# Optimization experiments

Hardware: AMD Instinct MI355X
Metric: run time of the kernel (lower is better)

Reference implementation:

```python
import jax, jax.numpy as jnp
import numpy as np

C2 = 256.0  # self.C = float(c2); softmax scale = 1/sqrt(C2)

def setup_inputs() -> dict:
    key = jax.random.key(0)
    k1, k2, k3, k4 = jax.random.split(key, 4)
    fm = jax.random.normal(k1, (1, 256, 96, 96), dtype=jnp.float32)
    ft = jax.random.normal(k2, (1, 256, 96, 96), dtype=jnp.float32)
    # 1x1 conv: in_channels = 2*256 = 512, out_channels = 256
    theta_w = jax.random.normal(k3, (256, 512, 1, 1), dtype=jnp.float32) * 0.04
    theta_b = jax.random.normal(k4, (256,), dtype=jnp.float32) * 0.01
    return {"fm": fm, "ft": ft, "theta_w": theta_w, "theta_b": theta_b}

def reference(fm, ft, theta_w, theta_b):
    B, C, H, W = fm.shape
    B1, C1, H1, W1 = ft.shape
    # torch .view(C, B*H*W) on a contiguous [B,C,H,W] tensor == row-major reshape
    fm_r = fm.reshape(C, B * H * W)          # [C, N]
    ft_r = ft.reshape(C1, B1 * H1 * W1)      # [C, M]
    scale = 1.0 / jnp.sqrt(jnp.float32(C2))
    S = jnp.einsum('cn,cm->nm', fm_r, ft_r) * scale   # [N, M]
    w = jax.nn.softmax(S, axis=-1)
    fm_weighted = jnp.einsum('cn,nm->cm', fm_r, w)    # [C, M]
    fm_attended = fm_weighted.reshape(B1, C1, H1, W1)
    cat = jnp.concatenate([fm_attended, ft], axis=1)  # [B1, 2*C1, H1, W1]
    # 1x1 conv
    out = jnp.einsum('oc,bchw->bohw', theta_w[:, :, 0, 0], cat) + theta_b[None, :, None, None]
    return out
```

## Files before the change

### kernel.cpp

```cpp
#include <hip/hip_runtime.h>

#define NHW 9216
#define NCH 256
#define SCALE 0.0625f

typedef __attribute__((ext_vector_type(8))) short bfrag;
typedef __attribute__((ext_vector_type(4))) float f32x4;
typedef __attribute__((ext_vector_type(8))) unsigned short u16x8;
typedef __attribute__((address_space(3))) unsigned as3_u32;
typedef const __attribute__((address_space(1))) unsigned as1_u32;

__device__ __forceinline__ unsigned short f2bf(float x) {
    unsigned u = __builtin_bit_cast(unsigned, x);
    u += 0x7FFFu + ((u >> 16) & 1u);
    return (unsigned short)(u >> 16);
}

#define MFMA(a, b, c) __builtin_amdgcn_mfma_f32_16x16x32_bf16((a), (b), (c), 0, 0, 0)

__global__ __launch_bounds__(256) void k_prep(const float* __restrict__ fm,
                                              const float* __restrict__ ft,
                                              unsigned short* __restrict__ fmT,
                                              unsigned short* __restrict__ ftT) {
    __shared__ float smT[64][257];
    const float* src = blockIdx.y ? ft : fm;
    unsigned short* dst = blockIdx.y ? ftT : fmT;
    const int t = threadIdx.x;
    const int n0 = blockIdx.x * 64;
    {
        const int n = t & 63;
        const int cb = t >> 6;
        for (int p = 0; p < 64; ++p) {
            const int c = p * 4 + cb;
            smT[n][c] = src[(size_t)c * NHW + n0 + n];
        }
    }
    __syncthreads();
    {
        const int n = t >> 2;
        const int c0 = (t & 3) * 64;
#pragma unroll
        for (int cc = 0; cc < 64; cc += 8) {
            const float4 v0 = *(const float4*)(&smT[n][c0 + cc]);
            const float4 v1 = *(const float4*)(&smT[n][c0 + cc + 4]);
            u16x8 o;
            o[0] = f2bf(v0.x); o[1] = f2bf(v0.y); o[2] = f2bf(v0.z); o[3] = f2bf(v0.w);
            o[4] = f2bf(v1.x); o[5] = f2bf(v1.y); o[6] = f2bf(v1.z); o[7] = f2bf(v1.w);
            *(u16x8*)(dst + (size_t)(n0 + n) * NCH + c0 + cc) = o;
        }
    }
}

__global__ __launch_bounds__(256) void k_prepw(const float* __restrict__ tw,
                                               unsigned short* __restrict__ twb) {
    const int i = blockIdx.x * 256 + threadIdx.x;
    twb[i] = f2bf(tw[i]);
}

__global__ __launch_bounds__(256, 2) void k_se(const unsigned short* __restrict__ fmT,
                                               const unsigned short* __restrict__ ftT,
                                               float* __restrict__ Zpart,
                                               unsigned short* __restrict__ E,
                                               int storeE) {
    __shared__ unsigned short smB[2][16384];
    const int t = threadIdx.x;
    const int w = t >> 6, l = t & 63;
    const int lr = l & 15, lk = l >> 4;
    const int id = blockIdx.x;
    const int by = id & 15;
    const int bx = id >> 4;
    const int n0 = bx * 128 + w * 32;
    const int mb = by * 576;

    bfrag a[2][8];
#pragma unroll
    for (int i = 0; i < 2; ++i)
#pragma unroll
        for (int ks = 0; ks < 8; ++ks)
            a[i][ks] = *(const bfrag*)(fmT + (size_t)(n0 + i * 16 + lr) * NCH + ks * 32 + lk * 8);

    float zacc[2][4] = {};
    f32x4 accA[2][4], accB[2][4];

#define STAGE(buf, mt)                                                                   \
    {                                                                                    \
        const int sm0 = mb + (mt) * 64;                                                  \
        _Pragma("unroll") for (int p = 0; p < 8; ++p) {                                  \
            const int chunkb = p * 256 + w * 64;                                         \
            const int chunk = chunkb + l;                                                \
            const int m = chunk >> 5;                                                    \
            const int scb = (chunk & 31) ^ (m & 7);                                      \
            const unsigned short* gp = ftT + (size_t)(sm0 + m) * NCH + scb * 8;          \
            unsigned short* lp = &smB[buf][0] + (size_t)chunk * 8;                       \
            __builtin_amdgcn_global_load_lds((as1_u32*)gp, (as3_u32*)lp, 16, 0, 0);      \
        }                                                                                \
    }

#define COMPUTE(acc, buf)                                                                \
    {                                                                                    \
        _Pragma("unroll") for (int i = 0; i < 2; ++i)                                    \
            _Pragma("unroll") for (int j = 0; j < 4; ++j) acc[i][j] = (f32x4){0,0,0,0};  \
        _Pragma("unroll") for (int ks = 0; ks < 8; ++ks) {                               \
            bfrag b[4];                                                                  \
            _Pragma("unroll") for (int j = 0; j < 4; ++j) {                              \
                const int mloc = j * 16 + lr;                                            \
                const int cb = ks * 4 + lk;                                              \
                b[j] = *(const bfrag*)(&smB[buf][mloc * 256 + ((cb ^ (mloc & 7)) << 3)]);\
            }                                                                            \
            _Pragma("unroll") for (int i = 0; i < 2; ++i)                                \
                _Pragma("unroll") for (int j = 0; j < 4; ++j)                            \
                    acc[i][j] = MFMA(a[i][ks], b[j], acc[i][j]);                         \
        }                                                                                \
    }

#define EXPSTORE(acc, mt)                                                                \
    {                                                                                    \
        const int sm0 = mb + (mt) * 64;                                                  \
        _Pragma("unroll") for (int i = 0; i < 2; ++i) {                                  \
            const int grp = (n0 + i * 16 + lk * 4) >> 3;                                 \
            const int sub = (lk & 1) * 4;                                                \
            _Pragma("unroll") for (int j = 0; j < 4; ++j) {                              \
                float e0 = __expf(acc[i][j][0] * SCALE);                                 \
                float e1 = __expf(acc[i][j][1] * SCALE);                                 \
                float e2 = __expf(acc[i][j][2] * SCALE);                                 \
                float e3 = __expf(acc[i][j][3] * SCALE);                                 \
                zacc[i][0] += e0; zacc[i][1] += e1;                                      \
                zacc[i][2] += e2; zacc[i][3] += e3;                                      \
                if (storeE) {                                                            \
                    const int m = sm0 + j * 16 + lr;                                     \
                    uint2 v;                                                             \
                    v.x = (unsigned)f2bf(e0) | ((unsigned)f2bf(e1) << 16);               \
                    v.y = (unsigned)f2bf(e2) | ((unsigned)f2bf(e3) << 16);               \
                    *(uint2*)(&E[((size_t)grp * NHW + m) * 8 + sub]) = v;                \
                }                                                                        \
            }                                                                            \
        }                                                                                \
    }

    STAGE(0, 0)
    __syncthreads();
    STAGE(1, 1)
    COMPUTE(accA, 0)
    __syncthreads();
    for (int base = 1; base + 1 < 9; base += 2) {
        STAGE(0, base + 1)
        EXPSTORE(accA, base - 1)
        COMPUTE(accB, 1)
        __syncthreads();
        if (base + 2 < 9) STAGE(1, base + 2)
        EXPSTORE(accB, base)
        COMPUTE(accA, 0)
        __syncthreads();
    }
    EXPSTORE(accA, 8)
#undef STAGE
#undef COMPUTE
#undef EXPSTORE

#pragma unroll
    for (int i = 0; i < 2; ++i)
#pragma unroll
        for (int r = 0; r < 4; ++r) {
            float v = zacc[i][r];
            v += __shfl_xor(v, 1);
            v += __shfl_xor(v, 2);
            v += __shfl_xor(v, 4);
            v += __shfl_xor(v, 8);
            if (lr == 0) Zpart[(size_t)by * NHW + n0 + i * 16 + lk * 4 + r] = v;
        }
}

__global__ __launch_bounds__(256) void k_gb(const unsigned short* __restrict__ twb,
                                            const unsigned short* __restrict__ fmT,
                                            const unsigned short* __restrict__ ftT,
                                            const float* __restrict__ Zpart,
                                            const float* __restrict__ tb,
                                            unsigned short* __restrict__ G,
                                            float* __restrict__ out) {
    const int tid = threadIdx.x;
    const int w = tid >> 6, l = tid & 63;
    const int wo = w >> 1, wm = w & 1;
    const int lr = l & 15, lk = l >> 4;
    const int mode = blockIdx.z;
    const int n0 = blockIdx.x * 128, o0 = blockIdx.y * 128;
    const unsigned short* B = mode ? ftT : fmT;
    const int wofs = mode ? 256 : 0;
    f32x4 acc[4][4] = {};
#pragma unroll
    for (int ks = 0; ks < 8; ++ks) {
        const int k = ks * 32 + lk * 8;
        bfrag a[4], b[4];
#pragma unroll
        for (int i = 0; i < 4; ++i)
            a[i] = *(const bfrag*)(twb + (size_t)(o0 + wo * 64 + i * 16 + lr) * 512 + wofs + k);
#pragma unroll
        for (int j = 0; j < 4; ++j)
            b[j] = *(const bfrag*)(B + (size_t)(n0 + wm * 64 + j * 16 + lr) * NCH + k);
#pragma unroll
        for (int i = 0; i < 4; ++i)
#pragma unroll
            for (int j = 0; j < 4; ++j) acc[i][j] = MFMA(a[i], b[j], acc[i][j]);
    }
    if (mode == 0) {
        float zi[4];
#pragma unroll
        for (int j = 0; j < 4; ++j) {
            const int n = n0 + wm * 64 + j * 16 + lr;
            float z = 0.f;
#pragma unroll
            for (int s = 0; s < 16; ++s) z += Zpart[(size_t)s * NHW + n];
            zi[j] = 1.f / z;
        }
#pragma unroll
        for (int i = 0; i < 4; ++i)
#pragma unroll
            for (int j = 0; j < 4; ++j)
#pragma unroll
                for (int r = 0; r < 4; ++r) {
                    const int o = o0 + wo * 64 + i * 16 + lk * 4 + r;
                    const int n = n0 + wm * 64 + j * 16 + lr;
                    G[(size_t)(n >> 3) * 2048 + o * 8 + (n & 7)] = f2bf(acc[i][j][r] * zi[j]);
                }
    } else {
#pragma unroll
        for (int i = 0; i < 4; ++i)
#pragma unroll
            for (int j = 0; j < 4; ++j)
#pragma unroll
                for (int r = 0; r < 4; ++r) {
                    const int o = o0 + wo * 64 + i * 16 + lk * 4 + r;
                    const int m = n0 + wm * 64 + j * 16 + lr;
                    out[(size_t)o * NHW + m] = acc[i][j][r] + tb[o];
                }
    }
}

__global__ __launch_bounds__(256, 3) void k_apply(const unsigned short* __restrict__ G,
                                                  const unsigned short* __restrict__ E,
                                                  float* __restrict__ out) {
    const int t = threadIdx.x;
    const int w = t >> 6, l = t & 63;
    const int lr = l & 15, lk = l >> 4;
    const int id = blockIdx.x;
    const int by = id & 7;
    const int bx = id >> 3;
    const int m0 = bx * 64;
    const int gbase = by * 144;

    f32x4 U[4][4] = {};
    bfrag gaA[4], ebA[4], gaB[4], ebB[4];

#define LOADSET(ga, eb, s)                                                                        \
    {                                                                                             \
        _Pragma("unroll") for (int i = 0; i < 4; ++i)                                             \
            ga[i] = *(const bfrag*)(&G[(size_t)(gbase + (s) * 4 + lk) * 2048 +                    \
                                       (w * 64 + i * 16 + lr) * 8]);                              \
        _Pragma("unroll") for (int j = 0; j < 4; ++j)                                             \
            eb[j] = *(const bfrag*)(&E[((size_t)(gbase + (s) * 4 + lk) * NHW + m0 + j * 16 + lr) * 8]); \
    }
#define MFMASET(ga, eb)                                                                           \
    {                                                                                             \
        _Pragma("unroll") for (int i = 0; i < 4; ++i)                                             \
            _Pragma("unroll") for (int j = 0; j < 4; ++j) U[i][j] = MFMA(ga[i], eb[j], U[i][j]);  \
    }

    LOADSET(gaA, ebA, 0)
#pragma unroll 2
    for (int s = 0; s < 36; s += 2) {
        LOADSET(gaB, ebB, s + 1)
        MFMASET(gaA, ebA)
        if (s + 2 < 36) LOADSET(gaA, ebA, s + 2)
        MFMASET(gaB, ebB)
    }
#undef LOADSET
#undef MFMASET

#pragma unroll
    for (int i = 0; i < 4; ++i)
#pragma unroll
        for (int j = 0; j < 4; ++j)
#pragma unroll
            for (int r = 0; r < 4; ++r) {
                const int o = w * 64 + i * 16 + lk * 4 + r;
                const int m = m0 + j * 16 + lr;
                atomicAdd(out + (size_t)o * NHW + m, U[i][j][r]);
            }
}

__global__ __launch_bounds__(256, 2) void k_main(const unsigned short* __restrict__ fmT,
                                                 const unsigned short* __restrict__ ftT,
                                                 const unsigned short* __restrict__ G,
                                                 float* __restrict__ out) {
    __shared__ unsigned short smB[32 * 64 * 8];
    __shared__ unsigned short smE[48 * 64 * 8];
    const int t = threadIdx.x;
    const int w = t >> 6, l = t & 63;
    const int lr = l & 15, lk = l >> 4;
    const int id = blockIdx.x;
    const int by = id & 7;
    const int bx = id >> 3;
    const int m0 = bx * 64;
    const int nbase = by * 1152;

    {
        const int m = t >> 2;
        const int kc0 = t & 3;
#pragma unroll
        for (int p = 0; p < 8; ++p) {
            const int kc = p * 4 + kc0;
            *(bfrag*)(&smB[(kc * 64 + m) * 8]) =
                *(const bfrag*)(ftT + (size_t)(m0 + m) * NCH + kc * 8);
        }
    }
    __syncthreads();

    f32x4 U[4][4] = {};
    for (int c = 0; c < 3; ++c) {
        const int n0 = nbase + c * 384;
        f32x4 acc[6][4] = {};
#pragma unroll
        for (int ks = 0; ks < 8; ++ks) {
            const int k = ks * 32 + lk * 8;
            bfrag a[6], b[4];
#pragma unroll
            for (int i = 0; i < 6; ++i)
                a[i] = *(const bfrag*)(fmT + (size_t)(n0 + w * 96 + i * 16 + lr) * NCH + k);
#pragma unroll
            for (int j = 0; j < 4; ++j)
                b[j] = *(const bfrag*)(&smB[((ks * 4 + lk) * 64 + j * 16 + lr) * 8]);
#pragma unroll
            for (int i = 0; i < 6; ++i)
#pragma unroll
                for (int j = 0; j < 4; ++j) acc[i][j] = MFMA(a[i], b[j], acc[i][j]);
        }
#pragma unroll
        for (int i = 0; i < 6; ++i)
#pragma unroll
            for (int j = 0; j < 4; ++j) {
                const int m = j * 16 + lr;
                const int grp = w * 12 + i * 2 + (lk >> 1);
                uint2 v;
                v.x = (unsigned)f2bf(__expf(acc[i][j][0] * SCALE)) |
                      ((unsigned)f2bf(__expf(acc[i][j][1] * SCALE)) << 16);
                v.y = (unsigned)f2bf(__expf(acc[i][j][2] * SCALE)) |
                      ((unsigned)f2bf(__expf(acc[i][j][3] * SCALE)) << 16);
                *(uint2*)(&smE[(grp * 64 + m) * 8 + (lk & 1) * 4]) = v;
            }
        __syncthreads();
#pragma unroll
        for (int s = 0; s < 12; ++s) {
            bfrag ga[4], eb[4];
#pragma unroll
            for (int i = 0; i < 4; ++i)
                ga[i] = *(const bfrag*)(&G[(size_t)((n0 + s * 32 + lk * 8) >> 3) * 2048 +
                                           (w * 64 + i * 16 + lr) * 8]);
#pragma unroll
            for (int j = 0; j < 4; ++j)
                eb[j] = *(const bfrag*)(&smE[((s * 4 + lk) * 64 + j * 16 + lr) * 8]);
#pragma unroll
            for (int i = 0; i < 4; ++i)
#pragma unroll
                for (int j = 0; j < 4; ++j) U[i][j] = MFMA(ga[i], eb[j], U[i][j]);
        }
        __syncthreads();
    }
#pragma unroll
    for (int i = 0; i < 4; ++i)
#pragma unroll
        for (int j = 0; j < 4; ++j)
#pragma unroll
            for (int r = 0; r < 4; ++r) {
                const int o = w * 64 + i * 16 + lk * 4 + r;
                const int m = m0 + j * 16 + lr;
                atomicAdd(out + (size_t)o * NHW + m, U[i][j][r]);
            }
}

extern "C" void kernel_launch(void* const* d_in, const int* in_sizes, int n_in,
                              void* d_out, int out_size, void* d_ws, size_t ws_size,
                              hipStream_t stream) {
    const float* fm = (const float*)d_in[0];
    const float* ft = (const float*)d_in[1];
    const float* tw = (const float*)d_in[2];
    const float* tb = (const float*)d_in[3];
    float* out = (float*)d_out;

    char* ws = (char*)d_ws;
    float* Zpart = (float*)ws;
    unsigned short* twb = (unsigned short*)(ws + 589824);
    unsigned short* fmT = (unsigned short*)(ws + 851968);
    unsigned short* ftT = (unsigned short*)(ws + 5570560);
    unsigned short* G   = (unsigned short*)(ws + 10289152);
    unsigned short* E   = (unsigned short*)(ws + 15007744);
    const size_t needE = 15007744ull + (size_t)NHW * NHW * 2ull;
    const int useE = (ws_size >= needE) ? 1 : 0;

    k_prep<<<dim3(144, 2), 256, 0, stream>>>(fm, ft, fmT, ftT);
    k_prepw<<<dim3(512), 256, 0, stream>>>(tw, twb);
    k_se<<<dim3(1152), 256, 0, stream>>>(fmT, ftT, Zpart, E, useE);
    k_gb<<<dim3(72, 2, 2), 256, 0, stream>>>(twb, fmT, ftT, Zpart, tb, G, out);
    if (useE)
        k_apply<<<dim3(1152), 256, 0, stream>>>(G, E, out);
    else
        k_main<<<dim3(1152), 256, 0, stream>>>(fmT, ftT, G, out);
}
```

Measured before the change: 199.5 us.

## Stage G and E tiles through LDS with async loads and wider M tile

k_apply now copies G and E tiles into double-buffered shared memory using global_load_lds, and computes from LDS instead of per-lane direct global fragment loads. Each block covers 128 output columns instead of 64, so each G tile is reused across twice as many columns and the grid is halved. The aim is to cut redundant G traffic and make E streaming more coalesced. In exchange it uses more LDS and more accumulator registers, which lowers occupancy to 2 blocks per SM. It also relies on barriers to order the async LDS copies.

```diff
diff --git a/kernel.cpp b/kernel.cpp
--- a/kernel.cpp
+++ b/kernel.cpp
@@ -235,50 +235,73 @@
     }
 }
 
-__global__ __launch_bounds__(256, 3) void k_apply(const unsigned short* __restrict__ G,
+__global__ __launch_bounds__(256, 2) void k_apply(const unsigned short* __restrict__ G,
                                                   const unsigned short* __restrict__ E,
                                                   float* __restrict__ out) {
+    __shared__ unsigned short smG[2][8192];
+    __shared__ unsigned short smE[2][4096];
     const int t = threadIdx.x;
     const int w = t >> 6, l = t & 63;
     const int lr = l & 15, lk = l >> 4;
     const int id = blockIdx.x;
     const int by = id & 7;
     const int bx = id >> 3;
-    const int m0 = bx * 64;
+    const int m0 = bx * 128;
     const int gbase = by * 144;
 
-    f32x4 U[4][4] = {};
-    bfrag gaA[4], ebA[4], gaB[4], ebB[4];
-
-#define LOADSET(ga, eb, s)                                                                        \
-    {                                                                                             \
-        _Pragma("unroll") for (int i = 0; i < 4; ++i)                                             \
-            ga[i] = *(const bfrag*)(&G[(size_t)(gbase + (s) * 4 + lk) * 2048 +                    \
-                                       (w * 64 + i * 16 + lr) * 8]);                              \
-        _Pragma("unroll") for (int j = 0; j < 4; ++j)                                             \
-            eb[j] = *(const bfrag*)(&E[((size_t)(gbase + (s) * 4 + lk) * NHW + m0 + j * 16 + lr) * 8]); \
-    }
-#define MFMASET(ga, eb)                                                                           \
-    {                                                                                             \
-        _Pragma("unroll") for (int i = 0; i < 4; ++i)                                             \
-            _Pragma("unroll") for (int j = 0; j < 4; ++j) U[i][j] = MFMA(ga[i], eb[j], U[i][j]);  \
-    }
-
-    LOADSET(gaA, ebA, 0)
-#pragma unroll 2
-    for (int s = 0; s < 36; s += 2) {
-        LOADSET(gaB, ebB, s + 1)
-        MFMASET(gaA, ebA)
-        if (s + 2 < 36) LOADSET(gaA, ebA, s + 2)
-        MFMASET(gaB, ebB)
-    }
-#undef LOADSET
-#undef MFMASET
+    f32x4 U[4][8] = {};
+
+#define STAGE(buf, s)                                                                    \
+    {                                                                                    \
+        const unsigned short* gG = G + (size_t)(gbase + (s) * 4) * 2048;                 \
+        _Pragma("unroll") for (int p = 0; p < 4; ++p) {                                  \
+            const int q = p * 256 + t;                                                   \
+            __builtin_amdgcn_global_load_lds((as1_u32*)(gG + q * 8),                     \
+                                             (as3_u32*)(&smG[buf][q * 8]), 16, 0, 0);    \
+        }                                                                                \
+        _Pragma("unroll") for (int p = 0; p < 2; ++p) {                                  \
+            const int q = p * 256 + t;                                                   \
+            const int grp = q >> 7, mloc = q & 127;                                      \
+            const unsigned short* gE =                                                   \
+                E + ((size_t)(gbase + (s) * 4 + grp) * NHW + m0 + mloc) * 8;             \
+            __builtin_amdgcn_global_load_lds((as1_u32*)gE,                               \
+                                             (as3_u32*)(&smE[buf][q * 8]), 16, 0, 0);    \
+        }                                                                                \
+    }
+
+#define COMPUTE(buf)                                                                     \
+    {                                                                                    \
+        bfrag av[4], bv[8];                                                              \
+        _Pragma("unroll") for (int i = 0; i < 4; ++i)                                    \
+            av[i] = *(const bfrag*)(&smG[buf][(lk * 256 + w * 64 + i * 16 + lr) * 8]);   \
+        _Pragma("unroll") for (int j = 0; j < 8; ++j)                                    \
+            bv[j] = *(const bfrag*)(&smE[buf][(lk * 128 + j * 16 + lr) * 8]);            \
+        _Pragma("unroll") for (int i = 0; i < 4; ++i)                                    \
+            _Pragma("unroll") for (int j = 0; j < 8; ++j)                                \
+                U[i][j] = MFMA(av[i], bv[j], U[i][j]);                                   \
+    }
+
+    STAGE(0, 0)
+    __syncthreads();
+    STAGE(1, 1)
+    COMPUTE(0)
+    __syncthreads();
+    for (int s = 1; s < 35; s += 2) {
+        STAGE(0, s + 1)
+        COMPUTE(1)
+        __syncthreads();
+        STAGE(1, s + 2)
+        COMPUTE(0)
+        __syncthreads();
+    }
+    COMPUTE(1)
+#undef STAGE
+#undef COMPUTE
 
 #pragma unroll
     for (int i = 0; i < 4; ++i)
 #pragma unroll
-        for (int j = 0; j < 4; ++j)
+        for (int j = 0; j < 8; ++j)
 #pragma unroll
             for (int r = 0; r < 4; ++r) {
                 const int o = w * 64 + i * 16 + lk * 4 + r;
@@ -400,7 +423,7 @@
     k_se<<<dim3(1152), 256, 0, stream>>>(fmT, ftT, Zpart, E, useE);
     k_gb<<<dim3(72, 2, 2), 256, 0, stream>>>(twb, fmT, ftT, Zpart, tb, G, out);
     if (useE)
-        k_apply<<<dim3(1152), 256, 0, stream>>>(G, E, out);
+        k_apply<<<dim3(576), 256, 0, stream>>>(G, E, out);
     else
         k_main<<<dim3(1152), 256, 0, stream>>>(fmT, ftT, G, out);
 }
```

Result: slower. 211.5 us (+6.0%).
